# Optimization experiments

Hardware: AMD Instinct MI355X
Metric: run time of the kernel (lower is better)

Reference implementation:

```python
import jax, jax.numpy as jnp
import numpy as np

B, N, C_IN, H, C_OUT = 8, 1024, 256, 4, 256
C = C_OUT // H  # per-head dim = 64
ALPHA = 0.2
NEG_INF = -9e15


def setup_inputs() -> dict:
    key = jax.random.key(0)
    k1, k2, k3, k4, k5 = jax.random.split(key, 5)
    node_feats = jax.random.normal(k1, (B, N, C_IN), dtype=jnp.float32)
    adj_matrix = jax.random.randint(k2, (B, N, N), 0, 2, dtype=jnp.int32)
    # include self-loops as GAT expects
    eye = jnp.eye(N, dtype=jnp.int32)[None]
    adj_matrix = jnp.maximum(adj_matrix, eye)
    # xavier_uniform with gain=1.414
    def xavier(k, shape, fan_in, fan_out, gain=1.414):
        lim = gain * np.sqrt(6.0 / (fan_in + fan_out))
        return jax.random.uniform(k, shape, jnp.float32, -lim, lim)
    W = xavier(k3, (C_OUT, C_IN), C_IN, C_OUT)          # projection weight [out,in]
    b = jnp.zeros((C_OUT,), dtype=jnp.float32)           # projection bias
    a = xavier(k4, (H, 2 * C), 2 * C, H)                 # attention vector per head
    return {"node_feats": node_feats, "adj_matrix": adj_matrix, "W": W, "b": b, "a": a}


def reference(node_feats, adj_matrix, W, b, a):
    Bb, Nn, _ = node_feats.shape
    Hh, twoC = a.shape
    Cc = twoC // 2
    # linear projection -> [B, N, H, C]
    h = (node_feats @ W.T + b).reshape(Bb, Nn, Hh, Cc)
    # edge logit(i,j) = leakyrelu(a . [h_i, h_j]) = leakyrelu(a1.h_i + a2.h_j)
    a_src, a_dst = a[:, :Cc], a[:, Cc:]
    l_src = jnp.einsum('bihc,hc->bih', h, a_src)  # [B,N,H]
    l_dst = jnp.einsum('bjhc,hc->bjh', h, a_dst)  # [B,N,H]
    logits = jax.nn.leaky_relu(l_src[:, :, None, :] + l_dst[:, None, :, :], ALPHA)  # [B,N,N,H]
    logits = jnp.where(adj_matrix[..., None] == 1, logits, NEG_INF)
    probs = jax.nn.softmax(logits, axis=2)  # softmax over neighbors j
    out = jnp.einsum('bijh,bjhc->bihc', probs, h)  # aggregate
    return out.reshape(Bb, Nn, Hh * Cc)  # concat heads
```

## Files before the change

kernel.cpp:

```cpp
#include <hip/hip_runtime.h>
#include <hip/hip_bf16.h>

#define BN   8
#define NN   1024
#define CIN  256
#define COUT 256
#define HH   4
#define CC   64
#define ALPHA_C 0.2f

typedef __attribute__((ext_vector_type(8))) short short8;
typedef __attribute__((ext_vector_type(4))) float f32x4;

__device__ __forceinline__ unsigned short f2bf(float x) {
    __hip_bfloat16 h = __float2bfloat16(x);
    return *(unsigned short*)&h;
}
__device__ __forceinline__ float bf2f(unsigned short u) {
    return __uint_as_float(((unsigned int)u) << 16);
}

__global__ __launch_bounds__(256) void k0_wpack(
    const float* __restrict__ W, unsigned short* __restrict__ Whp, unsigned short* __restrict__ Wlp)
{
    const int bid = blockIdx.x;
    const int n = threadIdx.x;
    const int fi = n * 64 + (bid >> 2) * 8 + (bid & 3) * 2;
    const float4* W4 = (const float4*)W;
    float4 wa = W4[fi], wb = W4[fi + 1];
    float xs[8] = {wa.x, wa.y, wa.z, wa.w, wb.x, wb.y, wb.z, wb.w};
    unsigned short hh[8], ll[8];
    #pragma unroll
    for (int e = 0; e < 8; ++e) {
        hh[e] = f2bf(xs[e]);
        ll[e] = f2bf(xs[e] - bf2f(hh[e]));
    }
    *(uint4*)(Whp + ((size_t)bid * 256 + n) * 8) = *(uint4*)hh;
    *(uint4*)(Wlp + ((size_t)bid * 256 + n) * 8) = *(uint4*)ll;
}

__global__ __launch_bounds__(256) void ka_adjpack(
    const int* __restrict__ adj, unsigned int* __restrict__ bmG)
{
    const int bid = blockIdx.x;
    const int b  = bid & 7;
    const int rl = bid >> 3;
    const int wv = threadIdx.x >> 6;
    const int l  = threadIdx.x & 63;
    const int row = b * NN + rl * 4 + wv;
    const int* arow = adj + (size_t)row * NN;
    #pragma unroll 4
    for (int it = 0; it < 16; ++it) {
        int av = arow[it * 64 + l];
        unsigned long long mb = __ballot(av != 0);
        if (l == 0) {
            bmG[row * 32 + 2 * it    ] = (unsigned int)mb;
            bmG[row * 32 + 2 * it + 1] = (unsigned int)(mb >> 32);
        }
    }
}

__global__ __launch_bounds__(1024, 1) void k1_gemm(
    const float* __restrict__ X, const float* __restrict__ bias, const float* __restrict__ a,
    const unsigned short* __restrict__ Whp, const unsigned short* __restrict__ Wlp,
    unsigned short* __restrict__ hbf_p, float* __restrict__ lsrc_t, float* __restrict__ ldst_t)
{
    __shared__ __align__(16) unsigned short Xh[32 * 256];
    __shared__ __align__(16) unsigned short Xl[32 * 256];
    __shared__ float lsP[2][8][2][16];

    const int bid = blockIdx.x;
    const int b  = bid & 7;
    const int tj = bid >> 3;
    const int row0 = b * NN + tj * 32;
    const int tid = threadIdx.x;
    const int wv = tid >> 6, l = tid & 63, il = l & 15, jg = l >> 4;
    const int mq = wv >> 3, no = wv & 7;

    {
        const float4* X4 = (const float4*)(X + (size_t)row0 * CIN);
        #pragma unroll
        for (int it = 0; it < 2; ++it) {
            int f = it * 1024 + tid;
            int r = f >> 6, k4 = f & 63;
            float4 x = X4[f];
            unsigned short h0 = f2bf(x.x), h1 = f2bf(x.y), h2 = f2bf(x.z), h3 = f2bf(x.w);
            unsigned short l0 = f2bf(x.x - bf2f(h0)), l1 = f2bf(x.y - bf2f(h1));
            unsigned short l2 = f2bf(x.z - bf2f(h2)), l3 = f2bf(x.w - bf2f(h3));
            unsigned short hs[4] = {h0, h1, h2, h3}, ls[4] = {l0, l1, l2, l3};
            int off = r * 512 + ((k4 * 8) ^ ((r & 7) << 4));
            *(uint2*)((char*)Xh + off) = *(uint2*)hs;
            *(uint2*)((char*)Xl + off) = *(uint2*)ls;
        }
    }
    __syncthreads();

    f32x4 acc0 = {0.f, 0.f, 0.f, 0.f}, acc1 = acc0;
    {
        const int abase = (mq * 16 + il) * 512;
        const int swz = (il & 7) << 4;
        const short8* Wh8 = (const short8*)Whp;
        const short8* Wl8 = (const short8*)Wlp;
        const int nb = no * 32 + il;
        #pragma unroll
        for (int kc = 0; kc < 8; ++kc) {
            const int ab = abase + ((kc * 64 + jg * 16) ^ swz);
            short8 Ah = *(const short8*)((const char*)Xh + ab);
            short8 Al = *(const short8*)((const char*)Xl + ab);
            const int pidx = (kc * 4 + jg) * 256 + nb;
            short8 Bh0 = Wh8[pidx],      Bl0 = Wl8[pidx];
            short8 Bh1 = Wh8[pidx + 16], Bl1 = Wl8[pidx + 16];
            acc0 = __builtin_amdgcn_mfma_f32_16x16x32_bf16(Ah, Bh0, acc0, 0, 0, 0);
            acc1 = __builtin_amdgcn_mfma_f32_16x16x32_bf16(Ah, Bh1, acc1, 0, 0, 0);
            acc0 = __builtin_amdgcn_mfma_f32_16x16x32_bf16(Ah, Bl0, acc0, 0, 0, 0);
            acc1 = __builtin_amdgcn_mfma_f32_16x16x32_bf16(Ah, Bl1, acc1, 0, 0, 0);
            acc0 = __builtin_amdgcn_mfma_f32_16x16x32_bf16(Al, Bh0, acc0, 0, 0, 0);
            acc1 = __builtin_amdgcn_mfma_f32_16x16x32_bf16(Al, Bh1, acc1, 0, 0, 0);
        }
    }

    const int c0 = no * 32 + il, c1 = c0 + 16;
    const float bia0 = bias[c0], bia1 = bias[c1];
    const int hh = no >> 1;
    const int cc0 = c0 & 63, cc1 = c1 & 63;
    const float as0 = a[hh * 128 + cc0],      as1 = a[hh * 128 + cc1];
    const float ad0 = a[hh * 128 + 64 + cc0], ad1 = a[hh * 128 + 64 + cc1];

    float v0[4], v1[4], psrc[4], pdst[4];
    #pragma unroll
    for (int r = 0; r < 4; ++r) {
        v0[r] = acc0[r] + bia0;
        v1[r] = acc1[r] + bia1;
        psrc[r] = v0[r] * as0 + v1[r] * as1;
        pdst[r] = v0[r] * ad0 + v1[r] * ad1;
    }
    #pragma unroll
    for (int off = 8; off >= 1; off >>= 1) {
        #pragma unroll
        for (int r = 0; r < 4; ++r) {
            psrc[r] += __shfl_xor(psrc[r], off);
            pdst[r] += __shfl_xor(pdst[r], off);
        }
    }
    __syncthreads();

    unsigned short* hp = Xh;
    #pragma unroll
    for (int r = 0; r < 4; ++r) {
        int m = mq * 16 + 4 * jg + r;
        int base = (m >> 3) * 128 + (m & 7);
        hp[(c0 >> 6) * 2048 + ((c0 & 63) >> 4) * 512 + base + (c0 & 15) * 8] = f2bf(v0[r]);
        hp[(c1 >> 6) * 2048 + ((c1 & 63) >> 4) * 512 + base + (c1 & 15) * 8] = f2bf(v1[r]);
    }
    if (il == 0) {
        #pragma unroll
        for (int r = 0; r < 4; ++r) {
            lsP[0][no][mq][4 * jg + r] = psrc[r];
            lsP[1][no][mq][4 * jg + r] = pdst[r];
        }
    }
    __syncthreads();

    {
        uint4* dst4 = (uint4*)(hbf_p + (size_t)(b * 32 + tj) * 8192);
        dst4[tid] = ((const uint4*)hp)[tid];
    }
    if (tid < 256) {
        int sd = tid >> 7, rem = tid & 127, h2 = rem >> 5, m = rem & 31;
        float v = lsP[sd][2 * h2][m >> 4][m & 15] + lsP[sd][2 * h2 + 1][m >> 4][m & 15];
        float* dst = sd ? ldst_t : lsrc_t;
        dst[((size_t)b * HH + h2) * NN + tj * 32 + m] = v;
    }
}

__global__ __launch_bounds__(1024, 2) void k2_attn(
    const unsigned short* __restrict__ hbf_p, const unsigned int* __restrict__ bmG,
    const float* __restrict__ lsrc_t, const float* __restrict__ ldst_t,
    float* __restrict__ out)
{
    __shared__ __align__(16) char smem[32768];
    __shared__ float lsumS[4][4][16];

    unsigned int (*adjw)[16] = (unsigned int (*)[16])smem;
    float* ldsTbl = (float*)(smem + 2048);

    const int bid = blockIdx.x;
    const int b  = bid & 7;
    const int i0 = (bid >> 3) * 16;
    const int tid = threadIdx.x;
    const int wv = tid >> 6, l = tid & 63, il = l & 15, jg = l >> 4;
    const int h = wv & 3, jh = wv >> 2;

    if (tid < 512) {
        const unsigned int* src = bmG + ((size_t)(b * NN + i0)) * 32;
        int row = tid >> 5, jw = tid & 31;
        adjw[jw][row] = src[row * 32 + jw];
    }
    ((float4*)ldsTbl)[tid] = ((const float4*)(ldst_t + (size_t)b * HH * NN))[tid];
    const float lsrc_v = lsrc_t[((size_t)b * HH + h) * NN + i0 + il];

    __syncthreads();

    float mx = -3.4e38f;
    #pragma unroll
    for (int jt = 0; jt < 16; ++jt) mx = fmaxf(mx, ldsTbl[h * 1024 + jt * 64 + l]);
    #pragma unroll
    for (int off = 32; off >= 1; off >>= 1) mx = fmaxf(mx, __shfl_xor(mx, off));
    const float t0  = lsrc_v + mx;
    const float m_r = fmaxf(t0, ALPHA_C * t0);
    float lsum = 0.f;

    f32x4 acc0 = {0.f,0.f,0.f,0.f}, acc1 = acc0, acc2 = acc0, acc3 = acc0;

    const short8* bfp = (const short8*)(hbf_p + (size_t)b * 32 * 8192);
    const int fb = h * 256 + l;
    const float* ltb = ldsTbl + h * 1024 + jg * 8;

    #pragma unroll 2
    for (int t = 0; t < 8; ++t) {
        const int tj = jh * 8 + t;
        short8 c0 = bfp[tj * 1024 + fb +   0];
        short8 c1 = bfp[tj * 1024 + fb +  64];
        short8 c2 = bfp[tj * 1024 + fb + 128];
        short8 c3 = bfp[tj * 1024 + fb + 192];
        const unsigned int bw = adjw[tj][il] >> (jg * 8);
        const float4 dA = *(const float4*)(ltb + tj * 32);
        const float4 dB = *(const float4*)(ltb + tj * 32 + 4);

        short8 af;
        #define PELEM(DV, E) {                                   \
            float s_ = lsrc_v + (DV);                            \
            s_ = fmaxf(s_, ALPHA_C * s_);                        \
            float p_ = __expf(s_ - m_r);                         \
            p_ = ((bw >> (E)) & 1u) ? p_ : 0.f;                  \
            lsum += p_;                                          \
            af[E] = (short)f2bf(p_); }
        PELEM(dA.x, 0) PELEM(dA.y, 1) PELEM(dA.z, 2) PELEM(dA.w, 3)
        PELEM(dB.x, 4) PELEM(dB.y, 5) PELEM(dB.z, 6) PELEM(dB.w, 7)
        #undef PELEM

        acc0 = __builtin_amdgcn_mfma_f32_16x16x32_bf16(af, c0, acc0, 0, 0, 0);
        acc1 = __builtin_amdgcn_mfma_f32_16x16x32_bf16(af, c1, acc1, 0, 0, 0);
        acc2 = __builtin_amdgcn_mfma_f32_16x16x32_bf16(af, c2, acc2, 0, 0, 0);
        acc3 = __builtin_amdgcn_mfma_f32_16x16x32_bf16(af, c3, acc3, 0, 0, 0);
    }

    lsum += __shfl_xor(lsum, 16);
    lsum += __shfl_xor(lsum, 32);
    if (l < 16) lsumS[jh][h][il] = lsum;
    __syncthreads();

    float* red = (float*)smem;
    float* rb = red + (jh & 1) * 4096;
    #define STOREALL(OP) {                                                    \
        const int base = (4 * jg) * 256 + h * 64 + il;                        \
        rb[base +   0 +  0] OP acc0[0]; rb[base +   0 + 16] OP acc1[0];       \
        rb[base +   0 + 32] OP acc2[0]; rb[base +   0 + 48] OP acc3[0];       \
        rb[base + 256 +  0] OP acc0[1]; rb[base + 256 + 16] OP acc1[1];       \
        rb[base + 256 + 32] OP acc2[1]; rb[base + 256 + 48] OP acc3[1];       \
        rb[base + 512 +  0] OP acc0[2]; rb[base + 512 + 16] OP acc1[2];       \
        rb[base + 512 + 32] OP acc2[2]; rb[base + 512 + 48] OP acc3[2];       \
        rb[base + 768 +  0] OP acc0[3]; rb[base + 768 + 16] OP acc1[3];       \
        rb[base + 768 + 32] OP acc2[3]; rb[base + 768 + 48] OP acc3[3]; }
    if (jh < 2) STOREALL(=)
    __syncthreads();
    if (jh >= 2) STOREALL(+=)
    __syncthreads();
    #undef STOREALL

    #pragma unroll
    for (int e = 0; e < 4; ++e) {
        int flat = e * 1024 + tid;
        int m = flat >> 8, c = flat & 255;
        int h2 = c >> 6;
        float v  = red[flat] + red[4096 + flat];
        float ls = lsumS[0][h2][m] + lsumS[1][h2][m] + lsumS[2][h2][m] + lsumS[3][h2][m];
        out[((size_t)(b * NN + i0 + m)) * COUT + c] = v / ls;
    }
}

extern "C" void kernel_launch(void* const* d_in, const int* in_sizes, int n_in,
                              void* d_out, int out_size, void* d_ws, size_t ws_size,
                              hipStream_t stream) {
    const float* X    = (const float*)d_in[0];
    const int*   adj  = (const int*)  d_in[1];
    const float* W    = (const float*)d_in[2];
    const float* bias = (const float*)d_in[3];
    const float* a    = (const float*)d_in[4];
    float* out = (float*)d_out;

    unsigned short* hbf_p = (unsigned short*)d_ws;
    float* lsrc_t = (float*)(hbf_p + (size_t)BN * 32 * 8192);
    float* ldst_t = lsrc_t + (size_t)BN * HH * NN;
    unsigned short* Whp = (unsigned short*)(ldst_t + (size_t)BN * HH * NN);
    unsigned short* Wlp = Whp + 65536;
    unsigned int*   bmG = (unsigned int*)(Wlp + 65536);

    k0_wpack<<<32, 256, 0, stream>>>(W, Whp, Wlp);
    ka_adjpack<<<(BN * NN) / 4, 256, 0, stream>>>(adj, bmG);
    k1_gemm<<<256, 1024, 0, stream>>>(X, bias, a, Whp, Wlp, hbf_p, lsrc_t, ldst_t);
    k2_attn<<<BN * (NN / 16), 1024, 0, stream>>>(hbf_p, bmG, lsrc_t, ldst_t, out);
}
```

Before: 46.94 us.

## Stage per-head h tile in LDS and process 128 rows per block

```diff
diff --git a/kernel.cpp b/kernel.cpp
--- a/kernel.cpp
+++ b/kernel.cpp
@@ -18,6 +18,11 @@
 }
 __device__ __forceinline__ float bf2f(unsigned short u) {
     return __uint_as_float(((unsigned int)u) << 16);
+}
+__device__ __forceinline__ void gl_lds16(const void* g, void* l) {
+    __builtin_amdgcn_global_load_lds(
+        (const __attribute__((address_space(1))) void*)g,
+        (__attribute__((address_space(3))) void*)l, 16, 0, 0);
 }
 
 __global__ __launch_bounds__(256) void k0_wpack(
@@ -173,63 +178,81 @@
     }
 }
 
-__global__ __launch_bounds__(1024, 2) void k2_attn(
+__global__ __launch_bounds__(1024, 1) void k2_attn(
     const unsigned short* __restrict__ hbf_p, const unsigned int* __restrict__ bmG,
     const float* __restrict__ lsrc_t, const float* __restrict__ ldst_t,
     float* __restrict__ out)
 {
-    __shared__ __align__(16) char smem[32768];
-    __shared__ float lsumS[4][4][16];
-
-    unsigned int (*adjw)[16] = (unsigned int (*)[16])smem;
-    float* ldsTbl = (float*)(smem + 2048);
+    __shared__ __align__(16) char smem[152576];
+    __shared__ float lsumS[8][2][16];
+
+    unsigned short* hS  = (unsigned short*)smem;
+    unsigned int*  bmS  = (unsigned int*)(smem + 131072);
+    float*        ldstS = (float*)(smem + 147712);
 
     const int bid = blockIdx.x;
     const int b  = bid & 7;
-    const int i0 = (bid >> 3) * 16;
+    const int hc = bid >> 3;
+    const int h  = hc & 3;
+    const int i0 = (hc >> 2) * 128;
     const int tid = threadIdx.x;
     const int wv = tid >> 6, l = tid & 63, il = l & 15, jg = l >> 4;
-    const int h = wv & 3, jh = wv >> 2;
-
-    if (tid < 512) {
-        const unsigned int* src = bmG + ((size_t)(b * NN + i0)) * 32;
-        int row = tid >> 5, jw = tid & 31;
-        adjw[jw][row] = src[row * 32 + jw];
-    }
-    ((float4*)ldsTbl)[tid] = ((const float4*)(ldst_t + (size_t)b * HH * NN))[tid];
-    const float lsrc_v = lsrc_t[((size_t)b * HH + h) * NN + i0 + il];
+    const int rg = wv >> 1, jhalf = wv & 1;
+
+    {
+        #pragma unroll
+        for (int k = 0; k < 2; ++k) {
+            const int tj = wv * 2 + k;
+            #pragma unroll
+            for (int cs = 0; cs < 4; ++cs) {
+                gl_lds16(hbf_p + ((((size_t)(b * 32 + tj)) * 1024 + h * 256 + cs * 64 + l) << 3),
+                         hS + (size_t)(tj * 256 + cs * 64 + l) * 8);
+            }
+        }
+    }
+    {
+        const unsigned int* bsrc = bmG + ((size_t)(b * NN + i0)) * 32;
+        #pragma unroll
+        for (int k = 0; k < 4; ++k) {
+            int idx = k * 1024 + tid;
+            int r = idx >> 5, w = idx & 31;
+            bmS[w * 130 + r] = bsrc[idx];
+        }
+    }
+    if (tid < 256)
+        ((float4*)ldstS)[tid] = ((const float4*)(ldst_t + ((size_t)(b * HH + h)) * NN))[tid];
+
+    const float lsv = lsrc_t[((size_t)(b * HH + h)) * NN + i0 + rg * 16 + il];
 
     __syncthreads();
 
     float mx = -3.4e38f;
     #pragma unroll
-    for (int jt = 0; jt < 16; ++jt) mx = fmaxf(mx, ldsTbl[h * 1024 + jt * 64 + l]);
+    for (int jt = 0; jt < 16; ++jt) mx = fmaxf(mx, ldstS[jt * 64 + l]);
     #pragma unroll
     for (int off = 32; off >= 1; off >>= 1) mx = fmaxf(mx, __shfl_xor(mx, off));
-    const float t0  = lsrc_v + mx;
+    const float t0  = lsv + mx;
     const float m_r = fmaxf(t0, ALPHA_C * t0);
     float lsum = 0.f;
 
     f32x4 acc0 = {0.f,0.f,0.f,0.f}, acc1 = acc0, acc2 = acc0, acc3 = acc0;
 
-    const short8* bfp = (const short8*)(hbf_p + (size_t)b * 32 * 8192);
-    const int fb = h * 256 + l;
-    const float* ltb = ldsTbl + h * 1024 + jg * 8;
+    const short8* hS8 = (const short8*)hS;
 
     #pragma unroll 2
-    for (int t = 0; t < 8; ++t) {
-        const int tj = jh * 8 + t;
-        short8 c0 = bfp[tj * 1024 + fb +   0];
-        short8 c1 = bfp[tj * 1024 + fb +  64];
-        short8 c2 = bfp[tj * 1024 + fb + 128];
-        short8 c3 = bfp[tj * 1024 + fb + 192];
-        const unsigned int bw = adjw[tj][il] >> (jg * 8);
-        const float4 dA = *(const float4*)(ltb + tj * 32);
-        const float4 dB = *(const float4*)(ltb + tj * 32 + 4);
+    for (int t = 0; t < 16; ++t) {
+        const int tj = jhalf * 16 + t;
+        short8 c0 = hS8[tj * 256 +   0 + l];
+        short8 c1 = hS8[tj * 256 +  64 + l];
+        short8 c2 = hS8[tj * 256 + 128 + l];
+        short8 c3 = hS8[tj * 256 + 192 + l];
+        const unsigned int bw = bmS[tj * 130 + rg * 16 + il] >> (jg * 8);
+        const float4 dA = *(const float4*)(ldstS + tj * 32 + jg * 8);
+        const float4 dB = *(const float4*)(ldstS + tj * 32 + jg * 8 + 4);
 
         short8 af;
         #define PELEM(DV, E) {                                   \
-            float s_ = lsrc_v + (DV);                            \
+            float s_ = lsv + (DV);                               \
             s_ = fmaxf(s_, ALPHA_C * s_);                        \
             float p_ = __expf(s_ - m_r);                         \
             p_ = ((bw >> (E)) & 1u) ? p_ : 0.f;                  \
@@ -247,35 +270,37 @@
 
     lsum += __shfl_xor(lsum, 16);
     lsum += __shfl_xor(lsum, 32);
-    if (l < 16) lsumS[jh][h][il] = lsum;
+    if (l < 16) lsumS[rg][jhalf][il] = lsum;
     __syncthreads();
 
     float* red = (float*)smem;
-    float* rb = red + (jh & 1) * 4096;
-    #define STOREALL(OP) {                                                    \
-        const int base = (4 * jg) * 256 + h * 64 + il;                        \
-        rb[base +   0 +  0] OP acc0[0]; rb[base +   0 + 16] OP acc1[0];       \
-        rb[base +   0 + 32] OP acc2[0]; rb[base +   0 + 48] OP acc3[0];       \
-        rb[base + 256 +  0] OP acc0[1]; rb[base + 256 + 16] OP acc1[1];       \
-        rb[base + 256 + 32] OP acc2[1]; rb[base + 256 + 48] OP acc3[1];       \
-        rb[base + 512 +  0] OP acc0[2]; rb[base + 512 + 16] OP acc1[2];       \
-        rb[base + 512 + 32] OP acc2[2]; rb[base + 512 + 48] OP acc3[2];       \
-        rb[base + 768 +  0] OP acc0[3]; rb[base + 768 + 16] OP acc1[3];       \
-        rb[base + 768 + 32] OP acc2[3]; rb[base + 768 + 48] OP acc3[3]; }
-    if (jh < 2) STOREALL(=)
-    __syncthreads();
-    if (jh >= 2) STOREALL(+=)
-    __syncthreads();
-    #undef STOREALL
-
-    #pragma unroll
-    for (int e = 0; e < 4; ++e) {
-        int flat = e * 1024 + tid;
-        int m = flat >> 8, c = flat & 255;
-        int h2 = c >> 6;
-        float v  = red[flat] + red[4096 + flat];
-        float ls = lsumS[0][h2][m] + lsumS[1][h2][m] + lsumS[2][h2][m] + lsumS[3][h2][m];
-        out[((size_t)(b * NN + i0 + m)) * COUT + c] = v / ls;
+    {
+        float* rb = red + (rg * 16 + 4 * jg) * 68 + il;
+        #define STOREALL(OP) {                                   \
+            rb[0 * 68 +  0] OP acc0[0]; rb[0 * 68 + 16] OP acc1[0]; \
+            rb[0 * 68 + 32] OP acc2[0]; rb[0 * 68 + 48] OP acc3[0]; \
+            rb[1 * 68 +  0] OP acc0[1]; rb[1 * 68 + 16] OP acc1[1]; \
+            rb[1 * 68 + 32] OP acc2[1]; rb[1 * 68 + 48] OP acc3[1]; \
+            rb[2 * 68 +  0] OP acc0[2]; rb[2 * 68 + 16] OP acc1[2]; \
+            rb[2 * 68 + 32] OP acc2[2]; rb[2 * 68 + 48] OP acc3[2]; \
+            rb[3 * 68 +  0] OP acc0[3]; rb[3 * 68 + 16] OP acc1[3]; \
+            rb[3 * 68 + 32] OP acc2[3]; rb[3 * 68 + 48] OP acc3[3]; }
+        if (jhalf == 0) STOREALL(=)
+        __syncthreads();
+        if (jhalf == 1) STOREALL(+=)
+        __syncthreads();
+        #undef STOREALL
+    }
+
+    #pragma unroll
+    for (int pass = 0; pass < 2; ++pass) {
+        int row = pass * 64 + (tid >> 4);
+        int c4  = tid & 15;
+        float4 v = *(const float4*)(red + row * 68 + c4 * 4);
+        float ls = lsumS[row >> 4][0][row & 15] + lsumS[row >> 4][1][row & 15];
+        float inv = 1.0f / ls;
+        float4 o = make_float4(v.x * inv, v.y * inv, v.z * inv, v.w * inv);
+        *(float4*)(out + ((size_t)(b * NN + i0 + row)) * COUT + h * 64 + c4 * 4) = o;
     }
 }
 
@@ -299,5 +324,5 @@
     k0_wpack<<<32, 256, 0, stream>>>(W, Whp, Wlp);
     ka_adjpack<<<(BN * NN) / 4, 256, 0, stream>>>(adj, bmG);
     k1_gemm<<<256, 1024, 0, stream>>>(X, bias, a, Whp, Wlp, hbf_p, lsrc_t, ldst_t);
-    k2_attn<<<BN * (NN / 16), 1024, 0, stream>>>(hbf_p, bmG, lsrc_t, ldst_t, out);
-}
+    k2_attn<<<256, 1024, 0, stream>>>(hbf_p, bmG, lsrc_t, ldst_t, out);
+}
```

Measured after the change: 45.49 us. 3.1% less time.
